# Kernel optimization log

Measured on AMD Instinct MI355X. Metric: run time of the kernel, lower is better.

Reference implementation:

```python
import jax, jax.numpy as jnp
import numpy as np

N, S, L, E, H = 8, 2, 512, 1024, 16
D = E // H  # head_dim = 64


def setup_inputs() -> dict:
    key = jax.random.key(0)
    ks = jax.random.split(key, 10)
    inp = {
        "values": jax.random.normal(ks[0], (N, S, L, E), dtype=jnp.float32),
        "keys": jax.random.normal(ks[1], (N, S, L, E), dtype=jnp.float32),
        "query": jax.random.normal(ks[2], (N, S, L, E), dtype=jnp.float32),
        "mask": jax.random.randint(ks[3], (N, S, L, 1), 0, 2, dtype=jnp.int32),
        # per-head projection weights, nn.Linear(D, D, bias=False): y = x @ W.T
        "Wv": jax.random.normal(ks[4], (D, D), dtype=jnp.float32) / np.sqrt(D),
        "Wk": jax.random.normal(ks[5], (D, D), dtype=jnp.float32) / np.sqrt(D),
        "Wq": jax.random.normal(ks[6], (D, D), dtype=jnp.float32) / np.sqrt(D),
        # output projection nn.Linear(E, E)
        "Wo": jax.random.normal(ks[7], (E, E), dtype=jnp.float32) / np.sqrt(E),
        "bo": jax.random.normal(ks[8], (E,), dtype=jnp.float32) * 0.01,
    }
    return inp


def reference(values, keys, query, mask, Wv, Wk, Wq, Wo, bo):
    n, s, l, e = query.shape
    h, d = H, D
    key_len = keys.shape[2]
    # split heads: (n, s, len, h, d)
    v = values.reshape(n, s, l, h, d) @ Wv.T
    k = keys.reshape(n, s, l, h, d) @ Wk.T
    q = query.reshape(n, s, l, h, d) @ Wq.T
    # energy: (n, s, h, q_len, k_len)
    energy = jnp.einsum('nsqhd,nskhd->nshqk', q, k)
    # mask[:, :, :, 0] masks QUERY positions (broadcast over heads and k)
    m = mask[:, :, :, 0]  # (n, s, l)
    energy = jnp.where(m[:, :, None, :, None] == 0, jnp.float32(-1e20), energy)
    # NOTE: softmax over the QUERY axis (dim=3), faithful to the original
    attn = jax.nn.softmax(energy / jnp.sqrt(jnp.float32(key_len)), axis=3)
    out = jnp.einsum('nshql,nslhd->nsqhd', attn, v)
    out = out.reshape(n, s, l, h * d)
    return out @ Wo.T + bo
```

## Files before the change

kernel.cpp:

```cpp
#include <hip/hip_runtime.h>
#include <math.h>

#define LL 512
#define EE 1024
#define HH 16
#define DD 64
#define NSX 16
#define NT (NSX*LL)
#define NSLE (NT*EE)
#define SCALE_Q 0.06375871f

typedef unsigned short u16;
typedef short bf16x8 __attribute__((ext_vector_type(8)));
typedef float f32x4 __attribute__((ext_vector_type(4)));

__device__ inline u16 f2bf(float f) {
  unsigned u = __float_as_uint(f);
  u += 0x7fff + ((u >> 16) & 1);
  return (u16)(u >> 16);
}

#define FEXP2(x) __builtin_amdgcn_exp2f(x)
#define MFMA32(a, b, c) __builtin_amdgcn_mfma_f32_16x16x32_bf16((a), (b), (c), 0, 0, 0)

__global__ void __launch_bounds__(256) convw_kernel(
    const float* __restrict__ Wv, const float* __restrict__ Wk,
    const float* __restrict__ Wq, const float* __restrict__ Wo,
    u16* __restrict__ Wvb, u16* __restrict__ Wkb,
    u16* __restrict__ Wqb, u16* __restrict__ Wob) {
  int i = blockIdx.x * 256 + threadIdx.x;
  const float* s; u16* d; int j;
  if (i < 262144) { s = Wo; d = Wob; j = i; }
  else {
    j = i - 262144;
    if (j < 1024)      { s = Wv; d = Wvb; }
    else if (j < 2048) { s = Wk; d = Wkb; j -= 1024; }
    else               { s = Wq; d = Wqb; j -= 2048; }
  }
  float4 f = ((const float4*)s)[j];
  ushort4 o; o.x = f2bf(f.x); o.y = f2bf(f.y); o.z = f2bf(f.z); o.w = f2bf(f.w);
  ((ushort4*)d)[j] = o;
}

__global__ void __launch_bounds__(256) proj_kernel(
    const float* __restrict__ vals, const float* __restrict__ keys,
    const float* __restrict__ qry,
    const u16* __restrict__ Wvb, const u16* __restrict__ Wkb,
    const u16* __restrict__ Wqb,
    u16* __restrict__ vpT, u16* __restrict__ kp, u16* __restrict__ qp) {
  const int b = blockIdx.x;
  const int h = b & 15, tt = (b >> 4) & 7, ns = (b >> 7) & 15, mat = b >> 11;
  const int tid = threadIdx.x;
  const float* src = (mat == 0 ? vals : mat == 1 ? keys : qry);
  const u16*   W   = (mat == 0 ? Wvb  : mat == 1 ? Wkb  : Wqb);
  __shared__ u16 xt[64][72];
  for (int i = tid; i < 1024; i += 256) {
    int t = i >> 4, dq = (i & 15) * 4;
    float4 f = *(const float4*)&src[((size_t)(ns*LL + tt*64 + t))*EE + h*DD + dq];
    ushort4 o; o.x = f2bf(f.x); o.y = f2bf(f.y); o.z = f2bf(f.z); o.w = f2bf(f.w);
    *(ushort4*)&xt[t][dq] = o;
  }
  __syncthreads();
  const int wid = tid >> 6, lane = tid & 63, quad = lane >> 4, l16 = lane & 15;
  bf16x8 a0 = *(const bf16x8*)&xt[wid*16 + l16][quad*8];
  bf16x8 a1 = *(const bf16x8*)&xt[wid*16 + l16][32 + quad*8];
  f32x4 z = {0.f, 0.f, 0.f, 0.f};
  f32x4 acc[4];
  #pragma unroll
  for (int nt = 0; nt < 4; ++nt) {
    bf16x8 b0 = *(const bf16x8*)&W[(nt*16 + l16)*DD + quad*8];
    bf16x8 b1 = *(const bf16x8*)&W[(nt*16 + l16)*DD + 32 + quad*8];
    acc[nt] = MFMA32(a0, b0, z);
    acc[nt] = MFMA32(a1, b1, acc[nt]);
  }
  if (mat == 0) {
    #pragma unroll
    for (int nt = 0; nt < 4; ++nt) {
      ushort4 o;
      o.x = f2bf(acc[nt][0]); o.y = f2bf(acc[nt][1]);
      o.z = f2bf(acc[nt][2]); o.w = f2bf(acc[nt][3]);
      size_t idx = ((size_t)((ns*HH + h)*DD + nt*16 + l16))*LL + tt*64 + wid*16 + quad*4;
      *(ushort4*)&vpT[idx] = o;
    }
  } else {
    u16* dst = (mat == 1 ? kp : qp);
    const float sc = (mat == 2) ? SCALE_Q : 1.f;
    __syncthreads();
    #pragma unroll
    for (int nt = 0; nt < 4; ++nt)
      #pragma unroll
      for (int r = 0; r < 4; ++r)
        xt[wid*16 + quad*4 + r][nt*16 + l16] = f2bf(acc[nt][r] * sc);
    __syncthreads();
    for (int i = tid; i < 512; i += 256) {
      int row = i >> 3, seg = (i & 7) * 8;
      *(bf16x8*)&dst[((size_t)(ns*LL + tt*64 + row))*EE + h*DD + seg] =
          *(const bf16x8*)&xt[row][seg];
    }
  }
}

__global__ void __launch_bounds__(1024, 4) attn_kernel(
    const u16* __restrict__ qp, const u16* __restrict__ kp,
    const u16* __restrict__ vpT, const int* __restrict__ mask,
    u16* __restrict__ oat) {
  const int b = blockIdx.x;
  const int h = b & 15, ns = b >> 4;
  const int tid = threadIdx.x;
  const int wid = tid >> 6, lane = tid & 63, quad = lane >> 4, l16 = lane & 15;
  __shared__ u16 Ks[LL][72];
  __shared__ u16 Vt[2][DD][72];
  __shared__ u16 pt[16][32][40];
  __shared__ float csum[LL];
  float* psum = (float*)pt;
  const size_t kgbase = ((size_t)(ns*LL))*EE + h*DD;
  for (int i = tid; i < 4096; i += 1024) {
    int row = i >> 3, seg = (i & 7) * 8;
    *(bf16x8*)&Ks[row][seg] = *(const bf16x8*)&kp[kgbase + (size_t)row*EE + seg];
  }
  const int q0 = wid*32;
  bf16x8 qf[2][2];
  float maf[2][4];
  #pragma unroll
  for (int qt = 0; qt < 2; ++qt) {
    const u16* qrow = qp + ((size_t)(ns*LL + q0 + qt*16 + l16))*EE + h*DD;
    qf[qt][0] = *(const bf16x8*)&qrow[quad*8];
    qf[qt][1] = *(const bf16x8*)&qrow[32 + quad*8];
    #pragma unroll
    for (int r = 0; r < 4; ++r)
      maf[qt][r] = mask[ns*LL + q0 + qt*16 + quad*4 + r] ? 1.f : 0.f;
  }
  f32x4 z = {0.f, 0.f, 0.f, 0.f};
  __syncthreads();
  for (int lt = 0; lt < 32; ++lt) {
    bf16x8 kf0 = *(const bf16x8*)&Ks[lt*16 + l16][quad*8];
    bf16x8 kf1 = *(const bf16x8*)&Ks[lt*16 + l16][32 + quad*8];
    float part = 0.f;
    #pragma unroll
    for (int qt = 0; qt < 2; ++qt) {
      f32x4 e = MFMA32(qf[qt][0], kf0, z);
      e = MFMA32(qf[qt][1], kf1, e);
      #pragma unroll
      for (int r = 0; r < 4; ++r)
        part += maf[qt][r] * FEXP2(e[r]);
    }
    part += __shfl_xor(part, 16);
    part += __shfl_xor(part, 32);
    if (quad == 0) psum[wid*512 + lt*16 + l16] = part;
  }
  __syncthreads();
  if (tid < LL) {
    float s = 0.f;
    #pragma unroll
    for (int w = 0; w < 16; ++w) s += psum[w*512 + tid];
    csum[tid] = (s > 0.f) ? 1.f/s : 0.f;
  }
  __syncthreads();
  f32x4 acc[4][2] = {{z,z},{z,z},{z,z},{z,z}};
  const size_t vgbase = ((size_t)((ns*HH + h)*DD))*LL;
  for (int lc = 0; lc < 8; ++lc) {
    if (tid < 512) {
      int row = tid >> 3, seg = (tid & 7) * 8;
      *(bf16x8*)&Vt[lc & 1][row][seg] =
          *(const bf16x8*)&vpT[vgbase + (size_t)row*LL + lc*64 + seg];
    }
    __syncthreads();
    #pragma unroll
    for (int lt2 = 0; lt2 < 4; ++lt2) {
      const int lrow = lc*64 + lt2*16 + l16;
      bf16x8 kf0 = *(const bf16x8*)&Ks[lrow][quad*8];
      bf16x8 kf1 = *(const bf16x8*)&Ks[lrow][32 + quad*8];
      const float csv = csum[lrow];
      #pragma unroll
      for (int qt = 0; qt < 2; ++qt) {
        f32x4 e = MFMA32(qf[qt][0], kf0, z);
        e = MFMA32(qf[qt][1], kf1, e);
        #pragma unroll
        for (int r = 0; r < 4; ++r)
          pt[wid][qt*16 + quad*4 + r][lt2 & 1 ? 16 + l16 : l16] =
              f2bf(maf[qt][r] * csv * FEXP2(e[r]));
        if (lt2 & 1) {
          bf16x8 pa = *(const bf16x8*)&pt[wid][qt*16 + l16][quad*8];
          #pragma unroll
          for (int dt = 0; dt < 4; ++dt) {
            bf16x8 vb = *(const bf16x8*)&Vt[lc & 1][dt*16 + l16]
                                        [(lt2 >> 1)*32 + quad*8];
            acc[dt][qt] = MFMA32(pa, vb, acc[dt][qt]);
          }
        }
      }
    }
  }
  #pragma unroll
  for (int qt = 0; qt < 2; ++qt)
    #pragma unroll
    for (int dt = 0; dt < 4; ++dt)
      #pragma unroll
      for (int r = 0; r < 4; ++r)
        oat[((size_t)(ns*LL + q0 + qt*16 + quad*4 + r))*EE + h*DD + dt*16 + l16] =
            f2bf(acc[dt][qt][r]);
}

__global__ void __launch_bounds__(256) out_gemm_kernel(
    const u16* __restrict__ A, const u16* __restrict__ Wob,
    const float* __restrict__ bo, float* __restrict__ Y) {
  __shared__ u16 As[128][72];
  __shared__ u16 Bs[128][72];
  const int b = blockIdx.x;
  const int nb = b & 7, mb = b >> 3;
  const int m0 = mb*128, n0 = nb*128;
  const int tid = threadIdx.x;
  const int wid = tid >> 6, lane = tid & 63, quad = lane >> 4, l16 = lane & 15;
  const int wm = (wid >> 1)*64, wn = (wid & 1)*64;
  f32x4 z = {0.f, 0.f, 0.f, 0.f};
  f32x4 acc[4][4];
  #pragma unroll
  for (int i = 0; i < 4; ++i)
    #pragma unroll
    for (int j = 0; j < 4; ++j) acc[i][j] = z;
  for (int k0 = 0; k0 < EE; k0 += 64) {
    __syncthreads();
    #pragma unroll
    for (int it = 0; it < 4; ++it) {
      int idx = it*256 + tid;
      int row = idx >> 3, seg = (idx & 7) * 8;
      *(bf16x8*)&As[row][seg] = *(const bf16x8*)&A  [(size_t)(m0 + row)*EE + k0 + seg];
      *(bf16x8*)&Bs[row][seg] = *(const bf16x8*)&Wob[(size_t)(n0 + row)*EE + k0 + seg];
    }
    __syncthreads();
    #pragma unroll
    for (int kk = 0; kk < 2; ++kk) {
      bf16x8 af[4], bfr[4];
      #pragma unroll
      for (int i = 0; i < 4; ++i)
        af[i] = *(const bf16x8*)&As[wm + i*16 + l16][kk*32 + quad*8];
      #pragma unroll
      for (int j = 0; j < 4; ++j)
        bfr[j] = *(const bf16x8*)&Bs[wn + j*16 + l16][kk*32 + quad*8];
      #pragma unroll
      for (int i = 0; i < 4; ++i)
        #pragma unroll
        for (int j = 0; j < 4; ++j)
          acc[i][j] = MFMA32(af[i], bfr[j], acc[i][j]);
    }
  }
  #pragma unroll
  for (int i = 0; i < 4; ++i)
    #pragma unroll
    for (int j = 0; j < 4; ++j) {
      int col = n0 + wn + j*16 + l16;
      float bias = bo[col];
      #pragma unroll
      for (int r = 0; r < 4; ++r)
        Y[(size_t)(m0 + wm + i*16 + quad*4 + r)*EE + col] = acc[i][j][r] + bias;
    }
}

extern "C" void kernel_launch(void* const* d_in, const int* in_sizes, int n_in,
                              void* d_out, int out_size, void* d_ws, size_t ws_size,
                              hipStream_t stream) {
  const float* values = (const float*)d_in[0];
  const float* keysp  = (const float*)d_in[1];
  const float* query  = (const float*)d_in[2];
  const int*   mask   = (const int*)d_in[3];
  const float* Wv = (const float*)d_in[4];
  const float* Wk = (const float*)d_in[5];
  const float* Wq = (const float*)d_in[6];
  const float* Wo = (const float*)d_in[7];
  const float* bo = (const float*)d_in[8];
  float* Y = (float*)d_out;

  u16* qp  = (u16*)d_ws;
  u16* kp  = qp + NSLE;
  u16* vpT = kp + NSLE;
  u16* oat = vpT + NSLE;
  u16* Wob = oat + NSLE;
  u16* Wvb = Wob + EE*EE;
  u16* Wkb = Wvb + DD*DD;
  u16* Wqb = Wkb + DD*DD;

  convw_kernel<<<1036, 256, 0, stream>>>(Wv, Wk, Wq, Wo, Wvb, Wkb, Wqb, Wob);
  proj_kernel<<<3*NSX*HH*(LL/64), 256, 0, stream>>>(values, keysp, query,
                                                    Wvb, Wkb, Wqb, vpT, kp, qp);
  attn_kernel<<<NSX*HH, 1024, 0, stream>>>(qp, kp, vpT, mask, oat);
  out_gemm_kernel<<<(NT/128)*(EE/128), 256, 0, stream>>>(oat, Wob, bo, Y);
}
```

Before: 236.4 us.

## Retile projection kernel to full-row 32-token tiles covering all heads

The projection kernel now has each block load a 32-token by 1024-element slab (all 16 heads) and keep the per-head weight fragments in registers. Each wave loops over 4 heads, so the grid shrinks from 6144 to 768 blocks. Global reads and the K/Q stores become contiguous full-row accesses instead of 128-byte head slices. The trade-offs are about 66KB of LDS per block, which lowers occupancy, and fewer blocks to spread across the CUs.

```diff
diff --git a/kernel.cpp b/kernel.cpp
--- a/kernel.cpp
+++ b/kernel.cpp
@@ -49,53 +49,74 @@
     const u16* __restrict__ Wqb,
     u16* __restrict__ vpT, u16* __restrict__ kp, u16* __restrict__ qp) {
   const int b = blockIdx.x;
-  const int h = b & 15, tt = (b >> 4) & 7, ns = (b >> 7) & 15, mat = b >> 11;
+  const int tt = b & 15, ns = (b >> 4) & 15, mat = b >> 8;
   const int tid = threadIdx.x;
   const float* src = (mat == 0 ? vals : mat == 1 ? keys : qry);
   const u16*   W   = (mat == 0 ? Wvb  : mat == 1 ? Wkb  : Wqb);
-  __shared__ u16 xt[64][72];
-  for (int i = tid; i < 1024; i += 256) {
-    int t = i >> 4, dq = (i & 15) * 4;
-    float4 f = *(const float4*)&src[((size_t)(ns*LL + tt*64 + t))*EE + h*DD + dq];
+  __shared__ u16 Xs[32][1032];
+  const size_t gbase = ((size_t)(ns*LL + tt*32))*EE;
+  #pragma unroll 8
+  for (int j = 0; j < 32; ++j) {
+    float4 f = *(const float4*)&src[gbase + (size_t)j*EE + tid*4];
     ushort4 o; o.x = f2bf(f.x); o.y = f2bf(f.y); o.z = f2bf(f.z); o.w = f2bf(f.w);
-    *(ushort4*)&xt[t][dq] = o;
-  }
+    *(ushort4*)&Xs[j][tid*4] = o;
+  }
+  const int wid = tid >> 6, lane = tid & 63, quad = lane >> 4, l16 = lane & 15;
+  bf16x8 wf[4][2];
+  #pragma unroll
+  for (int nt = 0; nt < 4; ++nt) {
+    wf[nt][0] = *(const bf16x8*)&W[(nt*16 + l16)*DD + quad*8];
+    wf[nt][1] = *(const bf16x8*)&W[(nt*16 + l16)*DD + 32 + quad*8];
+  }
+  f32x4 z = {0.f, 0.f, 0.f, 0.f};
   __syncthreads();
-  const int wid = tid >> 6, lane = tid & 63, quad = lane >> 4, l16 = lane & 15;
-  bf16x8 a0 = *(const bf16x8*)&xt[wid*16 + l16][quad*8];
-  bf16x8 a1 = *(const bf16x8*)&xt[wid*16 + l16][32 + quad*8];
-  f32x4 z = {0.f, 0.f, 0.f, 0.f};
-  f32x4 acc[4];
-  #pragma unroll
-  for (int nt = 0; nt < 4; ++nt) {
-    bf16x8 b0 = *(const bf16x8*)&W[(nt*16 + l16)*DD + quad*8];
-    bf16x8 b1 = *(const bf16x8*)&W[(nt*16 + l16)*DD + 32 + quad*8];
-    acc[nt] = MFMA32(a0, b0, z);
-    acc[nt] = MFMA32(a1, b1, acc[nt]);
-  }
-  if (mat == 0) {
-    #pragma unroll
-    for (int nt = 0; nt < 4; ++nt) {
-      ushort4 o;
-      o.x = f2bf(acc[nt][0]); o.y = f2bf(acc[nt][1]);
-      o.z = f2bf(acc[nt][2]); o.w = f2bf(acc[nt][3]);
-      size_t idx = ((size_t)((ns*HH + h)*DD + nt*16 + l16))*LL + tt*64 + wid*16 + quad*4;
-      *(ushort4*)&vpT[idx] = o;
-    }
-  } else {
+  const float sc = (mat == 2) ? SCALE_Q : 1.f;
+  #pragma unroll
+  for (int hh = 0; hh < 4; ++hh) {
+    const int h = wid*4 + hh;
+    bf16x8 af[2][2];
+    #pragma unroll
+    for (int m = 0; m < 2; ++m) {
+      af[m][0] = *(const bf16x8*)&Xs[m*16 + l16][h*DD + quad*8];
+      af[m][1] = *(const bf16x8*)&Xs[m*16 + l16][h*DD + 32 + quad*8];
+    }
+    f32x4 acc[2][4];
+    #pragma unroll
+    for (int m = 0; m < 2; ++m)
+      #pragma unroll
+      for (int nt = 0; nt < 4; ++nt) {
+        acc[m][nt] = MFMA32(af[m][0], wf[nt][0], z);
+        acc[m][nt] = MFMA32(af[m][1], wf[nt][1], acc[m][nt]);
+      }
+    if (mat == 0) {
+      #pragma unroll
+      for (int m = 0; m < 2; ++m)
+        #pragma unroll
+        for (int nt = 0; nt < 4; ++nt) {
+          ushort4 o;
+          o.x = f2bf(acc[m][nt][0]); o.y = f2bf(acc[m][nt][1]);
+          o.z = f2bf(acc[m][nt][2]); o.w = f2bf(acc[m][nt][3]);
+          size_t idx = ((size_t)((ns*HH + h)*DD + nt*16 + l16))*LL
+                       + tt*32 + m*16 + quad*4;
+          *(ushort4*)&vpT[idx] = o;
+        }
+    } else {
+      #pragma unroll
+      for (int m = 0; m < 2; ++m)
+        #pragma unroll
+        for (int nt = 0; nt < 4; ++nt)
+          #pragma unroll
+          for (int r = 0; r < 4; ++r)
+            Xs[m*16 + quad*4 + r][h*DD + nt*16 + l16] = f2bf(acc[m][nt][r] * sc);
+    }
+  }
+  if (mat != 0) {
     u16* dst = (mat == 1 ? kp : qp);
-    const float sc = (mat == 2) ? SCALE_Q : 1.f;
     __syncthreads();
     #pragma unroll
-    for (int nt = 0; nt < 4; ++nt)
-      #pragma unroll
-      for (int r = 0; r < 4; ++r)
-        xt[wid*16 + quad*4 + r][nt*16 + l16] = f2bf(acc[nt][r] * sc);
-    __syncthreads();
-    for (int i = tid; i < 512; i += 256) {
-      int row = i >> 3, seg = (i & 7) * 8;
-      *(bf16x8*)&dst[((size_t)(ns*LL + tt*64 + row))*EE + h*DD + seg] =
-          *(const bf16x8*)&xt[row][seg];
+    for (int i = tid; i < 4096; i += 256) {
+      int row = i >> 7, seg = (i & 127) * 8;
+      *(bf16x8*)&dst[gbase + (size_t)row*EE + seg] = *(const bf16x8*)&Xs[row][seg];
     }
   }
 }
@@ -280,8 +301,8 @@
   u16* Wqb = Wkb + DD*DD;
 
   convw_kernel<<<1036, 256, 0, stream>>>(Wv, Wk, Wq, Wo, Wvb, Wkb, Wqb, Wob);
-  proj_kernel<<<3*NSX*HH*(LL/64), 256, 0, stream>>>(values, keysp, query,
-                                                    Wvb, Wkb, Wqb, vpT, kp, qp);
+  proj_kernel<<<3*NSX*16, 256, 0, stream>>>(values, keysp, query,
+                                            Wvb, Wkb, Wqb, vpT, kp, qp);
   attn_kernel<<<NSX*HH, 1024, 0, stream>>>(qp, kp, vpT, mask, oat);
   out_gemm_kernel<<<(NT/128)*(EE/128), 256, 0, stream>>>(oat, Wob, bo, Y);
 }
```

Measured after the change: 229.7 us. 1.03x faster.

## Restructure projection kernel to keep weights in registers and skip LDS staging

Applied to the files above, without the earlier changes.

The projection kernel now assigns each block 16 tokens across all 16 heads, with each wave handling 4 heads. Each wave loads the per-head weight fragments into registers once and reuses them across those heads. Inputs are loaded straight from global memory into MFMA operand registers, so the LDS staging buffer and its barriers go away. The grid shrinks from 6144 to 1536 blocks. In exchange, K/Q outputs are written as scattered 2-byte stores instead of coalesced 16-byte stores, which may hurt write efficiency.

```diff
diff --git a/kernel.cpp b/kernel.cpp
--- a/kernel.cpp
+++ b/kernel.cpp
@@ -49,53 +49,60 @@
     const u16* __restrict__ Wqb,
     u16* __restrict__ vpT, u16* __restrict__ kp, u16* __restrict__ qp) {
   const int b = blockIdx.x;
-  const int h = b & 15, tt = (b >> 4) & 7, ns = (b >> 7) & 15, mat = b >> 11;
+  const int tt = b & 31, ns = (b >> 5) & 15, mat = b >> 9;
   const int tid = threadIdx.x;
+  const int wid = tid >> 6, lane = tid & 63, quad = lane >> 4, l16 = lane & 15;
   const float* src = (mat == 0 ? vals : mat == 1 ? keys : qry);
   const u16*   W   = (mat == 0 ? Wvb  : mat == 1 ? Wkb  : Wqb);
-  __shared__ u16 xt[64][72];
-  for (int i = tid; i < 1024; i += 256) {
-    int t = i >> 4, dq = (i & 15) * 4;
-    float4 f = *(const float4*)&src[((size_t)(ns*LL + tt*64 + t))*EE + h*DD + dq];
-    ushort4 o; o.x = f2bf(f.x); o.y = f2bf(f.y); o.z = f2bf(f.z); o.w = f2bf(f.w);
-    *(ushort4*)&xt[t][dq] = o;
-  }
-  __syncthreads();
-  const int wid = tid >> 6, lane = tid & 63, quad = lane >> 4, l16 = lane & 15;
-  bf16x8 a0 = *(const bf16x8*)&xt[wid*16 + l16][quad*8];
-  bf16x8 a1 = *(const bf16x8*)&xt[wid*16 + l16][32 + quad*8];
+  bf16x8 wf[4][2];
+  #pragma unroll
+  for (int nt = 0; nt < 4; ++nt) {
+    wf[nt][0] = *(const bf16x8*)&W[(nt*16 + l16)*DD + quad*8];
+    wf[nt][1] = *(const bf16x8*)&W[(nt*16 + l16)*DD + 32 + quad*8];
+  }
+  const int t0 = ns*LL + tt*16;
+  const float sc = (mat == 2) ? SCALE_Q : 1.f;
   f32x4 z = {0.f, 0.f, 0.f, 0.f};
-  f32x4 acc[4];
-  #pragma unroll
-  for (int nt = 0; nt < 4; ++nt) {
-    bf16x8 b0 = *(const bf16x8*)&W[(nt*16 + l16)*DD + quad*8];
-    bf16x8 b1 = *(const bf16x8*)&W[(nt*16 + l16)*DD + 32 + quad*8];
-    acc[nt] = MFMA32(a0, b0, z);
-    acc[nt] = MFMA32(a1, b1, acc[nt]);
-  }
-  if (mat == 0) {
+  u16* dst = (mat == 1 ? kp : qp);
+  #pragma unroll
+  for (int hh = 0; hh < 4; ++hh) {
+    const int h = wid*4 + hh;
+    const float* xrow = src + (size_t)(t0 + l16)*EE + h*DD;
+    float4 xa0 = *(const float4*)&xrow[quad*8];
+    float4 xa1 = *(const float4*)&xrow[quad*8 + 4];
+    float4 xb0 = *(const float4*)&xrow[32 + quad*8];
+    float4 xb1 = *(const float4*)&xrow[32 + quad*8 + 4];
+    bf16x8 af0, af1;
+    af0[0] = (short)f2bf(xa0.x); af0[1] = (short)f2bf(xa0.y);
+    af0[2] = (short)f2bf(xa0.z); af0[3] = (short)f2bf(xa0.w);
+    af0[4] = (short)f2bf(xa1.x); af0[5] = (short)f2bf(xa1.y);
+    af0[6] = (short)f2bf(xa1.z); af0[7] = (short)f2bf(xa1.w);
+    af1[0] = (short)f2bf(xb0.x); af1[1] = (short)f2bf(xb0.y);
+    af1[2] = (short)f2bf(xb0.z); af1[3] = (short)f2bf(xb0.w);
+    af1[4] = (short)f2bf(xb1.x); af1[5] = (short)f2bf(xb1.y);
+    af1[6] = (short)f2bf(xb1.z); af1[7] = (short)f2bf(xb1.w);
+    f32x4 acc[4];
     #pragma unroll
     for (int nt = 0; nt < 4; ++nt) {
-      ushort4 o;
-      o.x = f2bf(acc[nt][0]); o.y = f2bf(acc[nt][1]);
-      o.z = f2bf(acc[nt][2]); o.w = f2bf(acc[nt][3]);
-      size_t idx = ((size_t)((ns*HH + h)*DD + nt*16 + l16))*LL + tt*64 + wid*16 + quad*4;
-      *(ushort4*)&vpT[idx] = o;
-    }
-  } else {
-    u16* dst = (mat == 1 ? kp : qp);
-    const float sc = (mat == 2) ? SCALE_Q : 1.f;
-    __syncthreads();
-    #pragma unroll
-    for (int nt = 0; nt < 4; ++nt)
-      #pragma unroll
-      for (int r = 0; r < 4; ++r)
-        xt[wid*16 + quad*4 + r][nt*16 + l16] = f2bf(acc[nt][r] * sc);
-    __syncthreads();
-    for (int i = tid; i < 512; i += 256) {
-      int row = i >> 3, seg = (i & 7) * 8;
-      *(bf16x8*)&dst[((size_t)(ns*LL + tt*64 + row))*EE + h*DD + seg] =
-          *(const bf16x8*)&xt[row][seg];
+      acc[nt] = MFMA32(af0, wf[nt][0], z);
+      acc[nt] = MFMA32(af1, wf[nt][1], acc[nt]);
+    }
+    if (mat == 0) {
+      #pragma unroll
+      for (int nt = 0; nt < 4; ++nt) {
+        ushort4 o;
+        o.x = f2bf(acc[nt][0]); o.y = f2bf(acc[nt][1]);
+        o.z = f2bf(acc[nt][2]); o.w = f2bf(acc[nt][3]);
+        size_t idx = ((size_t)((ns*HH + h)*DD + nt*16 + l16))*LL + tt*16 + quad*4;
+        *(ushort4*)&vpT[idx] = o;
+      }
+    } else {
+      #pragma unroll
+      for (int nt = 0; nt < 4; ++nt)
+        #pragma unroll
+        for (int r = 0; r < 4; ++r)
+          dst[(size_t)(t0 + quad*4 + r)*EE + h*DD + nt*16 + l16] =
+              f2bf(acc[nt][r] * sc);
     }
   }
 }
@@ -280,8 +287,8 @@
   u16* Wqb = Wkb + DD*DD;
 
   convw_kernel<<<1036, 256, 0, stream>>>(Wv, Wk, Wq, Wo, Wvb, Wkb, Wqb, Wob);
-  proj_kernel<<<3*NSX*HH*(LL/64), 256, 0, stream>>>(values, keysp, query,
-                                                    Wvb, Wkb, Wqb, vpT, kp, qp);
+  proj_kernel<<<3*NSX*32, 256, 0, stream>>>(values, keysp, query,
+                                            Wvb, Wkb, Wqb, vpT, kp, qp);
   attn_kernel<<<NSX*HH, 1024, 0, stream>>>(qp, kp, vpT, mask, oat);
   out_gemm_kernel<<<(NT/128)*(EE/128), 256, 0, stream>>>(oat, Wob, bo, Y);
 }
```

Measured after the change: 232.0 us. No clear change (-1.9%).
